# Optimization experiments

Measured on AMD Instinct MI355X. Metric: run time of the kernel, lower is better.

Reference implementation:

```python
import jax, jax.numpy as jnp
import numpy as np

BATCH = 64
SEQ = 128
EMBED_DIM = 512
H = 1024
VOCAB = 32000


def setup_inputs() -> dict:
    key = jax.random.key(0)
    ks = jax.random.split(key, 10)
    prob = jax.random.randint(ks[0], (BATCH, SEQ), 0, VOCAB, dtype=jnp.int64)
    ans = jax.random.randint(ks[1], (BATCH,), 0, 10, dtype=jnp.int64)
    # nn.Embedding default init: N(0,1)
    embed_table = jax.random.normal(ks[2], (VOCAB, EMBED_DIM), jnp.float32)
    # nn.LSTMCell default init: U(-1/sqrt(h), 1/sqrt(h)), gates packed [i,f,g,o]
    k = 1.0 / np.sqrt(H).astype(np.float32)
    w_ih = jax.random.uniform(ks[3], (4 * H, EMBED_DIM), jnp.float32, -k, k)
    w_hh = jax.random.uniform(ks[4], (4 * H, H), jnp.float32, -k, k)
    b_ih = jax.random.uniform(ks[5], (4 * H,), jnp.float32, -k, k)
    b_hh = jax.random.uniform(ks[6], (4 * H,), jnp.float32, -k, k)
    # ansProj: Linear(h, 1)
    w_ans = jax.random.uniform(ks[7], (1, H), jnp.float32, -k, k)
    b_ans = jax.random.uniform(ks[7], (1,), jnp.float32, -k, k)
    # forward draws 0.01*randn initial states; pass them in for determinism
    h0 = 0.01 * jax.random.normal(ks[8], (BATCH, H), jnp.float32)
    c0 = 0.01 * jax.random.normal(ks[9], (BATCH, H), jnp.float32)
    return dict(prob=prob, ans=ans, embed_table=embed_table, w_ih=w_ih,
                w_hh=w_hh, b_ih=b_ih, b_hh=b_hh, w_ans=w_ans, b_ans=b_ans,
                h0=h0, c0=c0)


def reference(prob, ans, embed_table, w_ih, w_hh, b_ih, b_hh, w_ans, b_ans, h0, c0):
    del ans  # unpacked but unused in the original forward
    batch, seq = prob.shape
    num_unary = (seq - 2) // 2
    emb = embed_table[prob]                        # [B, S, E]
    xs = jnp.swapaxes(emb[:, :seq - 1], 0, 1)      # [T=S-1, B, E]

    def step(carry, x):
        h, c = carry
        gates = x @ w_ih.T + b_ih + h @ w_hh.T + b_hh   # [B, 4H]
        i, f, g, o = jnp.split(gates, 4, axis=-1)
        i = jax.nn.sigmoid(i)
        f = jax.nn.sigmoid(f)
        g = jnp.tanh(g)
        o = jax.nn.sigmoid(o)
        c = f * c + i * g
        h = o * jnp.tanh(c)
        return (h, c), h

    _, hs = jax.lax.scan(step, (h0, c0), xs)       # [T, B, H]
    preds = hs @ w_ans.T + b_ans                   # [T, B, 1]
    sel = preds[num_unary + 2:, :, 0]              # kept steps i > numUnary+1
    return sel.T                                   # [B, T-numUnary-2]
```

## Files before the change

kernel.cpp:

```cpp
#include <hip/hip_runtime.h>
#include <math.h>

#define BATCH   64
#define SEQLEN  128
#define EMBED   512
#define HID     1024
#define NSTEP   127
#define OUT0    65
#define NOUT    62

typedef unsigned short ushort_t;
typedef __attribute__((ext_vector_type(8))) __bf16 bf16x8;
typedef __attribute__((ext_vector_type(4))) float  f32x4;

__device__ __forceinline__ float sigmoidf_(float x) { return 1.f / (1.f + expf(-x)); }

__device__ __forceinline__ ushort_t f2bf(float f) {
    unsigned u = __builtin_bit_cast(unsigned, f);
    unsigned r = (u + 0x7FFFu + ((u >> 16) & 1u)) >> 16;
    return (ushort_t)r;
}
__device__ __forceinline__ float bf2f(ushort_t s) {
    unsigned u = ((unsigned)s) << 16;
    return __builtin_bit_cast(float, u);
}


__global__ __launch_bounds__(256) void init_mfma(
    const float* __restrict__ h0, const float* __restrict__ c0,
    float* __restrict__ cT, ushort_t* __restrict__ hf_hi, ushort_t* __restrict__ hf_lo)
{
    int id = blockIdx.x * 256 + threadIdx.x;
    int u = id >> 6, b = id & 63;
    cT[id] = c0[b * HID + u];
    float h = h0[b * HID + u];
    ushort_t hs = f2bf(h);
    ushort_t ls = f2bf(h - bf2f(hs));
    size_t idx = (((size_t)(u >> 5)) * 4 + (b >> 4)) * 512
               + ((((u & 31) >> 3) * 16) + (b & 15)) * 8 + (u & 7);
    hf_hi[idx] = hs;
    hf_lo[idx] = ls;
}

__global__ __launch_bounds__(256) void embed_frag(
    const int* __restrict__ prob, const float* __restrict__ embed,
    ushort_t* __restrict__ xf_hi, ushort_t* __restrict__ xf_lo)
{
    int t = blockIdx.x;
    for (int e = threadIdx.x; e < 64 * 512; e += 256) {
        int k = e & 511, b = e >> 9;
        int tok = prob[b * SEQLEN + t];
        float f = embed[(size_t)tok * EMBED + k];
        ushort_t hs = f2bf(f);
        ushort_t ls = f2bf(f - bf2f(hs));
        size_t idx = (((size_t)t * 16 + (k >> 5)) * 4 + (b >> 4)) * 512
                   + ((((k & 31) >> 3) * 16) + (b & 15)) * 8 + (k & 7);
        xf_hi[idx] = hs;
        xf_lo[idx] = ls;
    }
}

__global__ __launch_bounds__(512) void lstm_mfma(
    const ushort_t* __restrict__ xf_hi, const ushort_t* __restrict__ xf_lo,
    ushort_t* __restrict__ hf_hi, ushort_t* __restrict__ hf_lo,
    const float* __restrict__ cT,
    const float* __restrict__ w_ih, const float* __restrict__ w_hh,
    const float* __restrict__ b_ih, const float* __restrict__ b_hh,
    const float* __restrict__ w_ans, float* __restrict__ pout,
    int* __restrict__ bar)
{
    extern __shared__ ushort_t smem[];
    ushort_t* a_hi = smem;
    ushort_t* a_lo = smem + 48 * 512;
    float*    red  = (float*)(smem + 96 * 512);

    const int tid = threadIdx.x;
    const int bid = blockIdx.x;
    const int w   = tid >> 6;
    const int wn  = w & 3;
    const int kh  = w >> 2;
    const int L   = tid & 63;
    const int n   = L & 15;
    const int q   = L >> 4;
    const int u0  = bid * 4;
    const int ug  = u0 + q;
    const int bg  = wn * 16 + n;

    int* cnt  = bar + (bid & 7) * 32;
    int* scnt = bar + 256;
    int* go   = bar + 288;

    for (int m = 0; m < 16; ++m) {
        int unit = m >> 2, gate = m & 3;
        size_t rowg = (size_t)gate * HID + u0 + unit;
        #pragma unroll
        for (int i = 0; i < 3; ++i) {
            int k = tid + i * 512;
            float f = (k < EMBED) ? w_ih[rowg * EMBED + k]
                                  : w_hh[rowg * HID + (k - EMBED)];
            ushort_t hs = f2bf(f);
            ushort_t ls = f2bf(f - bf2f(hs));
            int off = (k >> 5) * 512 + (((k & 31) >> 3) * 16 + m) * 8 + (k & 7);
            a_hi[off] = hs;
            a_lo[off] = ls;
        }
    }

    float c = cT[ug * 64 + bg];
    float bs[4];
    #pragma unroll
    for (int j = 0; j < 4; ++j) bs[j] = b_ih[j * HID + ug] + b_hh[j * HID + ug];
    const float wansu = w_ans[ug];
    __syncthreads();

    for (int t = 0; t < NSTEP; ++t) {
        f32x4 acc = {0.f, 0.f, 0.f, 0.f};

        {
            const ushort_t* xh = xf_hi + (((size_t)t * 16 + kh * 8) * 4 + wn) * 512 + L * 8;
            const ushort_t* xl = xf_lo + (((size_t)t * 16 + kh * 8) * 4 + wn) * 512 + L * 8;
            bf16x8 bh = *(const bf16x8*)(xh);
            bf16x8 bl = *(const bf16x8*)(xl);
            #pragma unroll
            for (int ks = 0; ks < 8; ++ks) {
                bf16x8 bh1, bl1;
                if (ks < 7) {
                    bh1 = *(const bf16x8*)(xh + (size_t)(ks + 1) * 2048);
                    bl1 = *(const bf16x8*)(xl + (size_t)(ks + 1) * 2048);
                }
                bf16x8 ah = *(const bf16x8*)(a_hi + (kh * 8 + ks) * 512 + L * 8);
                bf16x8 al = *(const bf16x8*)(a_lo + (kh * 8 + ks) * 512 + L * 8);
                acc = __builtin_amdgcn_mfma_f32_16x16x32_bf16(ah, bh, acc, 0, 0, 0);
                acc = __builtin_amdgcn_mfma_f32_16x16x32_bf16(al, bh, acc, 0, 0, 0);
                acc = __builtin_amdgcn_mfma_f32_16x16x32_bf16(ah, bl, acc, 0, 0, 0);
                bh = bh1; bl = bl1;
            }
        }

        if (t > 0) {
            while (__hip_atomic_load(go, __ATOMIC_RELAXED,
                                     __HIP_MEMORY_SCOPE_AGENT) < t)
                __builtin_amdgcn_s_sleep(1);
            __builtin_amdgcn_fence(__ATOMIC_ACQUIRE, "workgroup");
        }

        {
            const ushort_t* hh = hf_hi + (((size_t)t * 32 + kh * 16) * 4 + wn) * 512 + L * 8;
            const ushort_t* hl = hf_lo + (((size_t)t * 32 + kh * 16) * 4 + wn) * 512 + L * 8;
            bf16x8 bh = *(const bf16x8*)(hh);
            bf16x8 bl = *(const bf16x8*)(hl);
            #pragma unroll
            for (int ks = 0; ks < 16; ++ks) {
                bf16x8 bh1, bl1;
                if (ks < 15) {
                    bh1 = *(const bf16x8*)(hh + (size_t)(ks + 1) * 2048);
                    bl1 = *(const bf16x8*)(hl + (size_t)(ks + 1) * 2048);
                }
                bf16x8 ah = *(const bf16x8*)(a_hi + (16 + kh * 16 + ks) * 512 + L * 8);
                bf16x8 al = *(const bf16x8*)(a_lo + (16 + kh * 16 + ks) * 512 + L * 8);
                acc = __builtin_amdgcn_mfma_f32_16x16x32_bf16(ah, bh, acc, 0, 0, 0);
                acc = __builtin_amdgcn_mfma_f32_16x16x32_bf16(al, bh, acc, 0, 0, 0);
                acc = __builtin_amdgcn_mfma_f32_16x16x32_bf16(ah, bl, acc, 0, 0, 0);
                bh = bh1; bl = bl1;
            }
        }

        if (w >= 4)
            *(f32x4*)(red + ((w - 4) * 64 + L) * 4) = acc;
        __syncthreads();

        if (w < 4) {
            f32x4 r = *(const f32x4*)(red + (w * 64 + L) * 4);
            acc += r;

            float ig = sigmoidf_(acc[0] + bs[0]);
            float fg = sigmoidf_(acc[1] + bs[1]);
            float gg = tanhf    (acc[2] + bs[2]);
            float og = sigmoidf_(acc[3] + bs[3]);
            c = fg * c + ig * gg;
            float h_new = og * tanhf(c);

            float p = h_new * wansu;
            p += __shfl_xor(p, 16, 64);
            p += __shfl_xor(p, 32, 64);
            if (t >= OUT0 && q == 0)
                pout[((size_t)(t - OUT0) * 256 + bid) * 64 + bg] = p;

            ushort_t hs = f2bf(h_new);
            ushort_t ls = f2bf(h_new - bf2f(hs));
            int kq = ug & 31, hks = ug >> 5;
            size_t idx = (((size_t)(t + 1) * 32 + hks) * 4 + wn) * 512
                       + (((kq >> 3) * 16) + n) * 8 + (kq & 7);
            __hip_atomic_store(&hf_hi[idx], hs, __ATOMIC_RELAXED,
                               __HIP_MEMORY_SCOPE_AGENT);
            __hip_atomic_store(&hf_lo[idx], ls, __ATOMIC_RELAXED,
                               __HIP_MEMORY_SCOPE_AGENT);
        }

        if (t == NSTEP - 1) break;

        __syncthreads();
        if (tid == 0) {
            int r = __hip_atomic_fetch_add(cnt, 1, __ATOMIC_RELAXED,
                                           __HIP_MEMORY_SCOPE_AGENT);
            if (r == 32 * (t + 1) - 1) {
                int s2 = __hip_atomic_fetch_add(scnt, 1, __ATOMIC_RELAXED,
                                                __HIP_MEMORY_SCOPE_AGENT);
                if (s2 == 8 * (t + 1) - 1)
                    __hip_atomic_store(go, t + 1, __ATOMIC_RELAXED,
                                       __HIP_MEMORY_SCOPE_AGENT);
            }
        }
    }
}

__global__ __launch_bounds__(256) void finalize_mfma(
    const float* __restrict__ pout, const float* __restrict__ b_ans,
    float* __restrict__ out)
{
    __shared__ float r[256];
    int col = blockIdx.x;
    int tid = threadIdx.x;
    int b = tid & 63, qq = tid >> 6;
    float s = 0.f;
    for (int i = qq; i < 256; i += 4)
        s += pout[((size_t)col * 256 + i) * 64 + b];
    r[tid] = s;
    __syncthreads();
    if (tid < 64)
        out[tid * NOUT + col] = r[tid] + r[64 + tid] + r[128 + tid] + r[192 + tid]
                              + b_ans[0];
}

#define NBLK    512
#define NTHR    512
#define REDA_OFF 12288
#define REDB_OFF 14336
#define REDC_OFF 15360
#define C_OFF    15872
#define HEAD_OFF 16000
#define LDS_FLOATS 16128

__global__ __launch_bounds__(256) void init_state(
    const float* __restrict__ h0, const float* __restrict__ c0,
    float* __restrict__ hT, float* __restrict__ cT)
{
    int id = blockIdx.x * 256 + threadIdx.x;
    int u = id >> 6, b = id & 63;
    hT[id] = h0[b * HID + u];
    cT[id] = c0[b * HID + u];
}

__global__ __launch_bounds__(256) void embed_transpose(
    const int* __restrict__ prob, const float* __restrict__ embed,
    float* __restrict__ xT)
{
    __shared__ float xe[64 * 132];
    int t = blockIdx.x;
    int tid = threadIdx.x;
    for (int kt = 0; kt < 4; ++kt) {
        #pragma unroll
        for (int i = 0; i < 8; ++i) {
            int id = tid + i * 256;
            int b  = id >> 5;
            int k4 = id & 31;
            int tok = prob[b * SEQLEN + t];
            float4 v = *(const float4*)(embed + (size_t)tok * EMBED + kt * 128 + k4 * 4);
            *(float4*)(&xe[b * 132 + k4 * 4]) = v;
        }
        __syncthreads();
        #pragma unroll
        for (int i = 0; i < 8; ++i) {
            int id = tid + i * 256;
            int kl = id >> 4;
            int b4 = id & 15;
            float4 v;
            v.x = xe[(b4 * 4 + 0) * 132 + kl];
            v.y = xe[(b4 * 4 + 1) * 132 + kl];
            v.z = xe[(b4 * 4 + 2) * 132 + kl];
            v.w = xe[(b4 * 4 + 3) * 132 + kl];
            *(float4*)(&xT[((size_t)t * EMBED + kt * 128 + kl) * 64 + b4 * 4]) = v;
        }
        __syncthreads();
    }
}

__global__ __launch_bounds__(NTHR, 4) void lstm_persist_hist(
    const float* __restrict__ xT, float* __restrict__ h_hist,
    const float* __restrict__ cT,
    const float* __restrict__ w_ih, const float* __restrict__ w_hh,
    const float* __restrict__ b_ih, const float* __restrict__ b_hh,
    const float* __restrict__ w_ans, float* __restrict__ pout,
    int* __restrict__ bar)
{
    __shared__ float lds[LDS_FLOATS];
    const int tid = threadIdx.x;
    const int bid = blockIdx.x;
    const int b   = tid & 63;
    const int ksl = __builtin_amdgcn_readfirstlane(tid >> 6);
    const int u0  = bid * 2;

    int* sliceCnt = bar + (bid >> 6) * 32;
    int* mySlice  = bar + 256 + (bid >> 6) * 32;
    int* waitGo   = bar + 256 + ksl * 32;

    for (int idx = tid; idx < 12288; idx += NTHR) {
        int r  = idx / 1536;
        int k  = idx - r * 1536;
        int u2 = r & 1, gate = r >> 1;
        int row = gate * HID + u0 + u2;
        float v = (k < EMBED) ? w_ih[(size_t)row * EMBED + k]
                              : w_hh[(size_t)row * HID + (k - EMBED)];
        lds[(u2 * 1536 + k) * 4 + gate] = v;
    }
    if (tid < 128) lds[C_OFF + tid] = cT[u0 * 64 + tid];

    float bias[2][4], wans[2];
    #pragma unroll
    for (int uu = 0; uu < 2; ++uu) {
        #pragma unroll
        for (int j = 0; j < 4; ++j) {
            int rj = j * HID + u0 + uu;
            bias[uu][j] = b_ih[rj] + b_hh[rj];
        }
        wans[uu] = w_ans[u0 + uu];
    }
    __syncthreads();

    for (int t = 0; t < NSTEP; ++t) {
        const float* xt = xT + (size_t)t * EMBED * 64;
        const float* ht = h_hist + (size_t)t * HID * 64;
        float* hn_buf   = h_hist + (size_t)(t + 1) * HID * 64;

        float acc[2][4];
        #pragma unroll
        for (int uu = 0; uu < 2; ++uu)
            #pragma unroll
            for (int j = 0; j < 4; ++j) acc[uu][j] = 0.f;

        const int kx0 = ksl * 64;
        #pragma unroll 4
        for (int g = 0; g < 16; ++g) {
            const int k = kx0 + g * 4;
            float xv[4];
            #pragma unroll
            for (int i = 0; i < 4; ++i) xv[i] = xt[(size_t)(k + i) * 64 + b];
            #pragma unroll
            for (int i = 0; i < 4; ++i) {
                float4 wa = *(const float4*)&lds[(0 * 1536 + k + i) * 4];
                float4 wb = *(const float4*)&lds[(1 * 1536 + k + i) * 4];
                acc[0][0] = fmaf(wa.x, xv[i], acc[0][0]);
                acc[0][1] = fmaf(wa.y, xv[i], acc[0][1]);
                acc[0][2] = fmaf(wa.z, xv[i], acc[0][2]);
                acc[0][3] = fmaf(wa.w, xv[i], acc[0][3]);
                acc[1][0] = fmaf(wb.x, xv[i], acc[1][0]);
                acc[1][1] = fmaf(wb.y, xv[i], acc[1][1]);
                acc[1][2] = fmaf(wb.z, xv[i], acc[1][2]);
                acc[1][3] = fmaf(wb.w, xv[i], acc[1][3]);
            }
        }

        if (t > 0) {
            while (__hip_atomic_load(waitGo, __ATOMIC_RELAXED,
                                     __HIP_MEMORY_SCOPE_AGENT) < t)
                __builtin_amdgcn_s_sleep(4);
            __builtin_amdgcn_fence(__ATOMIC_ACQUIRE, "workgroup");
        }

        const int kh0 = ksl * 128;
        #pragma unroll 4
        for (int g = 0; g < 32; ++g) {
            const int kh = kh0 + g * 4;
            float hv[4];
            #pragma unroll
            for (int i = 0; i < 4; ++i)
                hv[i] = ht[(size_t)(kh + i) * 64 + b];
            #pragma unroll
            for (int i = 0; i < 4; ++i) {
                const int kw = EMBED + kh + i;
                float4 wa = *(const float4*)&lds[(0 * 1536 + kw) * 4];
                float4 wb = *(const float4*)&lds[(1 * 1536 + kw) * 4];
                acc[0][0] = fmaf(wa.x, hv[i], acc[0][0]);
                acc[0][1] = fmaf(wa.y, hv[i], acc[0][1]);
                acc[0][2] = fmaf(wa.z, hv[i], acc[0][2]);
                acc[0][3] = fmaf(wa.w, hv[i], acc[0][3]);
                acc[1][0] = fmaf(wb.x, hv[i], acc[1][0]);
                acc[1][1] = fmaf(wb.y, hv[i], acc[1][1]);
                acc[1][2] = fmaf(wb.z, hv[i], acc[1][2]);
                acc[1][3] = fmaf(wb.w, hv[i], acc[1][3]);
            }
        }

        if (ksl >= 4) {
            #pragma unroll
            for (int uu = 0; uu < 2; ++uu)
                #pragma unroll
                for (int j = 0; j < 4; ++j)
                    lds[REDA_OFF + (((ksl - 4) * 8) + uu * 4 + j) * 64 + b] = acc[uu][j];
        }
        __syncthreads();
        if (ksl < 4) {
            #pragma unroll
            for (int uu = 0; uu < 2; ++uu)
                #pragma unroll
                for (int j = 0; j < 4; ++j)
                    acc[uu][j] += lds[REDA_OFF + ((ksl * 8) + uu * 4 + j) * 64 + b];
        }
        if (ksl == 2 || ksl == 3) {
            #pragma unroll
            for (int uu = 0; uu < 2; ++uu)
                #pragma unroll
                for (int j = 0; j < 4; ++j)
                    lds[REDB_OFF + (((ksl - 2) * 8) + uu * 4 + j) * 64 + b] = acc[uu][j];
        }
        __syncthreads();
        if (ksl < 2) {
            #pragma unroll
            for (int uu = 0; uu < 2; ++uu)
                #pragma unroll
                for (int j = 0; j < 4; ++j)
                    acc[uu][j] += lds[REDB_OFF + ((ksl * 8) + uu * 4 + j) * 64 + b];
        }
        if (ksl == 0) {
            #pragma unroll
            for (int j = 0; j < 4; ++j)
                lds[REDC_OFF + j * 64 + b] = acc[1][j];
        }
        if (ksl == 1) {
            #pragma unroll
            for (int j = 0; j < 4; ++j)
                lds[REDC_OFF + (4 + j) * 64 + b] = acc[0][j];
        }
        __syncthreads();
        if (ksl < 2) {
            const int uu = ksl;
            float s[4];
            if (ksl == 0) {
                #pragma unroll
                for (int j = 0; j < 4; ++j)
                    s[j] = acc[0][j] + lds[REDC_OFF + (4 + j) * 64 + b];
            } else {
                #pragma unroll
                for (int j = 0; j < 4; ++j)
                    s[j] = acc[1][j] + lds[REDC_OFF + j * 64 + b];
            }
            float i_g = sigmoidf_(s[0] + bias[uu][0]);
            float f_g = sigmoidf_(s[1] + bias[uu][1]);
            float g_g = tanhf   (s[2] + bias[uu][2]);
            float o_g = sigmoidf_(s[3] + bias[uu][3]);
            float c_old = lds[C_OFF + uu * 64 + b];
            float c_new = f_g * c_old + i_g * g_g;
            float h_new = o_g * tanhf(c_new);
            lds[C_OFF + uu * 64 + b] = c_new;
            __hip_atomic_store(&hn_buf[(u0 + uu) * 64 + b], h_new,
                               __ATOMIC_RELAXED, __HIP_MEMORY_SCOPE_AGENT);
            lds[HEAD_OFF + uu * 64 + b] = h_new * wans[uu];
        }

        __syncthreads();
        if (t >= OUT0 && tid < 64) {
            pout[((size_t)(t - OUT0) * NBLK + bid) * 64 + tid] =
                lds[HEAD_OFF + tid] + lds[HEAD_OFF + 64 + tid];
        }
        if (t == NSTEP - 1) break;
        if (tid == 0) {
            int r = __hip_atomic_fetch_add(sliceCnt, 1, __ATOMIC_RELAXED,
                                           __HIP_MEMORY_SCOPE_AGENT);
            if (r == 64 * (t + 1) - 1)
                __hip_atomic_store(mySlice, t + 1, __ATOMIC_RELAXED,
                                   __HIP_MEMORY_SCOPE_AGENT);
        }
    }
}

__global__ __launch_bounds__(256) void finalize_persist(
    const float* __restrict__ pout, const float* __restrict__ b_ans,
    float* __restrict__ out)
{
    __shared__ float r[256];
    int col = blockIdx.x;
    int tid = threadIdx.x;
    int b = tid & 63, qq = tid >> 6;
    float s = 0.f;
    for (int i = qq; i < NBLK; i += 4)
        s += pout[((size_t)col * NBLK + i) * 64 + b];
    r[tid] = s;
    __syncthreads();
    if (tid < 64)
        out[tid * NOUT + col] = r[tid] + r[64 + tid] + r[128 + tid] + r[192 + tid]
                              + b_ans[0];
}

extern "C" void kernel_launch(void* const* d_in, const int* in_sizes, int n_in,
                              void* d_out, int out_size, void* d_ws, size_t ws_size,
                              hipStream_t stream)
{
    const int*   prob  = (const int*)  d_in[0];
    const float* embed = (const float*)d_in[2];
    const float* w_ih  = (const float*)d_in[3];
    const float* w_hh  = (const float*)d_in[4];
    const float* b_ih  = (const float*)d_in[5];
    const float* b_hh  = (const float*)d_in[6];
    const float* w_ans = (const float*)d_in[7];
    const float* b_ans = (const float*)d_in[8];
    const float* h0    = (const float*)d_in[9];
    const float* c0    = (const float*)d_in[10];

    char* W = (char*)d_ws;
    float*    cT_m  = (float*)   (W);
    float*    poutm = (float*)   (W + 262144);
    ushort_t* xf_hi = (ushort_t*)(W + 4325376);
    ushort_t* xf_lo = (ushort_t*)(W + 12648448);
    ushort_t* hf_hi = (ushort_t*)(W + 20971520);
    ushort_t* hf_lo = (ushort_t*)(W + 37748736);
    int*      bar_m = (int*)     (W + 54525952);

    const int DYN_LDS = 96 * 1024 + 4096;

    hipError_t err = hipFuncSetAttribute(
        (const void*)lstm_mfma,
        hipFuncAttributeMaxDynamicSharedMemorySize, DYN_LDS);

    if (err == hipSuccess) {
        hipMemsetAsync(bar_m, 0, 2048, stream);
        init_mfma<<<256, 256, 0, stream>>>(h0, c0, cT_m, hf_hi, hf_lo);
        embed_frag<<<NSTEP, 256, 0, stream>>>(prob, embed, xf_hi, xf_lo);

        void* args[] = {
            (void*)&xf_hi, (void*)&xf_lo, (void*)&hf_hi, (void*)&hf_lo,
            (void*)&cT_m, (void*)&w_ih, (void*)&w_hh, (void*)&b_ih,
            (void*)&b_hh, (void*)&w_ans, (void*)&poutm, (void*)&bar_m
        };
        err = hipLaunchCooperativeKernel((const void*)lstm_mfma,
                                         dim3(256), dim3(512),
                                         args, DYN_LDS, stream);
        if (err == hipSuccess) {
            finalize_mfma<<<NOUT, 256, 0, stream>>>(poutm, b_ans, (float*)d_out);
            return;
        }
    }

    float* ws     = (float*)d_ws;
    float* cT     = ws;
    float* pout   = ws + 65536;
    float* xT     = ws + 2097152;
    float* h_hist = ws + 6258688;
    int*   bar    = (int*)(ws + 14647296);

    hipMemsetAsync(bar, 0, 2048, stream);
    init_state<<<256, 256, 0, stream>>>(h0, c0, h_hist, cT);
    embed_transpose<<<NSTEP, 256, 0, stream>>>(prob, embed, xT);

    void* args9[] = {
        (void*)&xT, (void*)&h_hist, (void*)&cT,
        (void*)&w_ih, (void*)&w_hh, (void*)&b_ih, (void*)&b_hh,
        (void*)&w_ans, (void*)&pout, (void*)&bar
    };
    hipLaunchCooperativeKernel((const void*)lstm_persist_hist,
                               dim3(NBLK), dim3(NTHR), args9, 0, stream);
    finalize_persist<<<NOUT, 256, 0, stream>>>(pout, b_ans, (float*)d_out);
}
```

Baseline: 911.1 us.

## Split LSTM step K-reduction across 16 waves and vectorize embedding fragment packing

The persistent LSTM kernel goes from 512 to 1024 threads per block, so four wave groups each handle a quarter of the K dimension instead of two groups taking half. This halves the serial MFMA chain per wave on the latency-bound recurrent step. The partial sums are combined by a two-stage LDS reduction with an extra barrier and more LDS space. Separately, the embedding packing kernel now loads 8 floats at a time and writes bf16x8 vectors instead of scalar stores.

```diff
diff --git a/kernel.cpp b/kernel.cpp
--- a/kernel.cpp
+++ b/kernel.cpp
@@ -47,20 +47,31 @@
     ushort_t* __restrict__ xf_hi, ushort_t* __restrict__ xf_lo)
 {
     int t = blockIdx.x;
-    for (int e = threadIdx.x; e < 64 * 512; e += 256) {
-        int k = e & 511, b = e >> 9;
+    for (int e = threadIdx.x; e < 4096; e += 256) {
+        int b  = e >> 6;
+        int kb = e & 63;
+        int k  = kb * 8;
         int tok = prob[b * SEQLEN + t];
-        float f = embed[(size_t)tok * EMBED + k];
-        ushort_t hs = f2bf(f);
-        ushort_t ls = f2bf(f - bf2f(hs));
-        size_t idx = (((size_t)t * 16 + (k >> 5)) * 4 + (b >> 4)) * 512
-                   + ((((k & 31) >> 3) * 16) + (b & 15)) * 8 + (k & 7);
-        xf_hi[idx] = hs;
-        xf_lo[idx] = ls;
-    }
-}
-
-__global__ __launch_bounds__(512) void lstm_mfma(
+        const float* row = embed + (size_t)tok * EMBED + k;
+        float4 f0 = *(const float4*)(row);
+        float4 f1 = *(const float4*)(row + 4);
+        float fv[8] = { f0.x, f0.y, f0.z, f0.w, f1.x, f1.y, f1.z, f1.w };
+        bf16x8 hv, lv;
+        #pragma unroll
+        for (int i = 0; i < 8; ++i) {
+            ushort_t hs = f2bf(fv[i]);
+            ushort_t ls = f2bf(fv[i] - bf2f(hs));
+            hv[i] = __builtin_bit_cast(__bf16, hs);
+            lv[i] = __builtin_bit_cast(__bf16, ls);
+        }
+        size_t idx = (((size_t)t * 16 + (kb >> 2)) * 4 + (b >> 4)) * 512
+                   + (((kb & 3) * 16) + (b & 15)) * 8;
+        *(bf16x8*)(xf_hi + idx) = hv;
+        *(bf16x8*)(xf_lo + idx) = lv;
+    }
+}
+
+__global__ __launch_bounds__(1024) void lstm_mfma(
     const ushort_t* __restrict__ xf_hi, const ushort_t* __restrict__ xf_lo,
     ushort_t* __restrict__ hf_hi, ushort_t* __restrict__ hf_lo,
     const float* __restrict__ cT,
@@ -72,13 +83,14 @@
     extern __shared__ ushort_t smem[];
     ushort_t* a_hi = smem;
     ushort_t* a_lo = smem + 48 * 512;
-    float*    red  = (float*)(smem + 96 * 512);
+    float*    redA = (float*)(smem + 96 * 512);
+    float*    redB = redA + 2048;
 
     const int tid = threadIdx.x;
     const int bid = blockIdx.x;
     const int w   = tid >> 6;
     const int wn  = w & 3;
-    const int kh  = w >> 2;
+    const int kq  = w >> 2;
     const int L   = tid & 63;
     const int n   = L & 15;
     const int q   = L >> 4;
@@ -93,9 +105,7 @@
     for (int m = 0; m < 16; ++m) {
         int unit = m >> 2, gate = m & 3;
         size_t rowg = (size_t)gate * HID + u0 + unit;
-        #pragma unroll
-        for (int i = 0; i < 3; ++i) {
-            int k = tid + i * 512;
+        for (int k = tid; k < 1536; k += 1024) {
             float f = (k < EMBED) ? w_ih[rowg * EMBED + k]
                                   : w_hh[rowg * HID + (k - EMBED)];
             ushort_t hs = f2bf(f);
@@ -117,19 +127,19 @@
         f32x4 acc = {0.f, 0.f, 0.f, 0.f};
 
         {
-            const ushort_t* xh = xf_hi + (((size_t)t * 16 + kh * 8) * 4 + wn) * 512 + L * 8;
-            const ushort_t* xl = xf_lo + (((size_t)t * 16 + kh * 8) * 4 + wn) * 512 + L * 8;
+            const ushort_t* xh = xf_hi + (((size_t)t * 16 + kq * 4) * 4 + wn) * 512 + L * 8;
+            const ushort_t* xl = xf_lo + (((size_t)t * 16 + kq * 4) * 4 + wn) * 512 + L * 8;
             bf16x8 bh = *(const bf16x8*)(xh);
             bf16x8 bl = *(const bf16x8*)(xl);
             #pragma unroll
-            for (int ks = 0; ks < 8; ++ks) {
+            for (int ks = 0; ks < 4; ++ks) {
                 bf16x8 bh1, bl1;
-                if (ks < 7) {
+                if (ks < 3) {
                     bh1 = *(const bf16x8*)(xh + (size_t)(ks + 1) * 2048);
                     bl1 = *(const bf16x8*)(xl + (size_t)(ks + 1) * 2048);
                 }
-                bf16x8 ah = *(const bf16x8*)(a_hi + (kh * 8 + ks) * 512 + L * 8);
-                bf16x8 al = *(const bf16x8*)(a_lo + (kh * 8 + ks) * 512 + L * 8);
+                bf16x8 ah = *(const bf16x8*)(a_hi + (kq * 4 + ks) * 512 + L * 8);
+                bf16x8 al = *(const bf16x8*)(a_lo + (kq * 4 + ks) * 512 + L * 8);
                 acc = __builtin_amdgcn_mfma_f32_16x16x32_bf16(ah, bh, acc, 0, 0, 0);
                 acc = __builtin_amdgcn_mfma_f32_16x16x32_bf16(al, bh, acc, 0, 0, 0);
                 acc = __builtin_amdgcn_mfma_f32_16x16x32_bf16(ah, bl, acc, 0, 0, 0);
@@ -145,19 +155,19 @@
         }
 
         {
-            const ushort_t* hh = hf_hi + (((size_t)t * 32 + kh * 16) * 4 + wn) * 512 + L * 8;
-            const ushort_t* hl = hf_lo + (((size_t)t * 32 + kh * 16) * 4 + wn) * 512 + L * 8;
+            const ushort_t* hh = hf_hi + (((size_t)t * 32 + kq * 8) * 4 + wn) * 512 + L * 8;
+            const ushort_t* hl = hf_lo + (((size_t)t * 32 + kq * 8) * 4 + wn) * 512 + L * 8;
             bf16x8 bh = *(const bf16x8*)(hh);
             bf16x8 bl = *(const bf16x8*)(hl);
             #pragma unroll
-            for (int ks = 0; ks < 16; ++ks) {
+            for (int ks = 0; ks < 8; ++ks) {
                 bf16x8 bh1, bl1;
-                if (ks < 15) {
+                if (ks < 7) {
                     bh1 = *(const bf16x8*)(hh + (size_t)(ks + 1) * 2048);
                     bl1 = *(const bf16x8*)(hl + (size_t)(ks + 1) * 2048);
                 }
-                bf16x8 ah = *(const bf16x8*)(a_hi + (16 + kh * 16 + ks) * 512 + L * 8);
-                bf16x8 al = *(const bf16x8*)(a_lo + (16 + kh * 16 + ks) * 512 + L * 8);
+                bf16x8 ah = *(const bf16x8*)(a_hi + (16 + kq * 8 + ks) * 512 + L * 8);
+                bf16x8 al = *(const bf16x8*)(a_lo + (16 + kq * 8 + ks) * 512 + L * 8);
                 acc = __builtin_amdgcn_mfma_f32_16x16x32_bf16(ah, bh, acc, 0, 0, 0);
                 acc = __builtin_amdgcn_mfma_f32_16x16x32_bf16(al, bh, acc, 0, 0, 0);
                 acc = __builtin_amdgcn_mfma_f32_16x16x32_bf16(ah, bl, acc, 0, 0, 0);
@@ -165,12 +175,19 @@
             }
         }
 
-        if (w >= 4)
-            *(f32x4*)(red + ((w - 4) * 64 + L) * 4) = acc;
-        __syncthreads();
-
-        if (w < 4) {
-            f32x4 r = *(const f32x4*)(red + (w * 64 + L) * 4);
+        if (kq >= 2)
+            *(f32x4*)(redA + ((w - 8) * 64 + L) * 4) = acc;
+        __syncthreads();
+        if (kq < 2) {
+            f32x4 r = *(const f32x4*)(redA + (w * 64 + L) * 4);
+            acc += r;
+        }
+        if (kq == 1)
+            *(f32x4*)(redB + ((w - 4) * 64 + L) * 4) = acc;
+        __syncthreads();
+
+        if (kq == 0) {
+            f32x4 r = *(const f32x4*)(redB + (w * 64 + L) * 4);
             acc += r;
 
             float ig = sigmoidf_(acc[0] + bs[0]);
@@ -188,9 +205,9 @@
 
             ushort_t hs = f2bf(h_new);
             ushort_t ls = f2bf(h_new - bf2f(hs));
-            int kq = ug & 31, hks = ug >> 5;
+            int kr = ug & 31, hks = ug >> 5;
             size_t idx = (((size_t)(t + 1) * 32 + hks) * 4 + wn) * 512
-                       + (((kq >> 3) * 16) + n) * 8 + (kq & 7);
+                       + (((kr >> 3) * 16) + n) * 8 + (kr & 7);
             __hip_atomic_store(&hf_hi[idx], hs, __ATOMIC_RELAXED,
                                __HIP_MEMORY_SCOPE_AGENT);
             __hip_atomic_store(&hf_lo[idx], ls, __ATOMIC_RELAXED,
@@ -515,7 +532,7 @@
     ushort_t* hf_lo = (ushort_t*)(W + 37748736);
     int*      bar_m = (int*)     (W + 54525952);
 
-    const int DYN_LDS = 96 * 1024 + 4096;
+    const int DYN_LDS = 96 * 1024 + 12288;
 
     hipError_t err = hipFuncSetAttribute(
         (const void*)lstm_mfma,
@@ -532,7 +549,7 @@
             (void*)&b_hh, (void*)&w_ans, (void*)&poutm, (void*)&bar_m
         };
         err = hipLaunchCooperativeKernel((const void*)lstm_mfma,
-                                         dim3(256), dim3(512),
+                                         dim3(256), dim3(1024),
                                          args, DYN_LDS, stream);
         if (err == hipSuccess) {
             finalize_mfma<<<NOUT, 256, 0, stream>>>(poutm, b_ans, (float*)d_out);
```

Result: no change. 902.5 us (-0.9%).
